# Performance work log

Hardware: AMD Instinct MI355X
Metric: run time of the kernel (lower is better)

## Reference

```python
import jax, jax.numpy as jnp
import numpy as np

WIN = 9  # window_size (isotropic, module default)
EPS = 1e-5


def _box_sum3d(x, win):
    """Sum over a win^3 box, same-size output ('same' padding). x: [B,1,D,H,W].
    The ones kernel is separable, so apply three 1D convolutions."""
    pad = win // 2
    for ax in range(3):  # spatial axes D,H,W
        kshape = [1, 1, 1, 1, 1]
        kshape[2 + ax] = win
        k = jnp.ones(kshape, x.dtype)
        padding = [(0, 0)] * 3
        padding[ax] = (pad, pad)
        x = jax.lax.conv_general_dilated(x, k, window_strides=(1, 1, 1), padding=padding)
    return x


def setup_inputs() -> dict:
    key = jax.random.key(0)
    k1, k2 = jax.random.split(key)
    shape = (2, 1, 160, 192, 160)
    y_pred = jax.random.normal(k1, shape, dtype=jnp.float32)
    y_true = jax.random.normal(k2, shape, dtype=jnp.float32)
    return {"y_pred": y_pred, "y_true": y_true}


def reference(y_pred, y_true):
    I, J = y_true, y_pred
    win_size = jnp.asarray(WIN ** 3, I.dtype)  # 729

    I_sum = _box_sum3d(I, WIN)
    J_sum = _box_sum3d(J, WIN)
    I2_sum = _box_sum3d(I * I, WIN)
    J2_sum = _box_sum3d(J * J, WIN)
    IJ_sum = _box_sum3d(I * J, WIN)

    I_mean = I_sum / win_size
    J_mean = J_sum / win_size

    cross = IJ_sum - J_mean * I_sum - I_mean * J_sum + I_mean * J_mean * win_size
    I_var = I2_sum - 2 * I_mean * I_sum + I_mean * I_mean * win_size
    J_var = J2_sum - 2 * J_mean * J_sum + J_mean * J_mean * win_size

    cc = cross * cross / (I_var * J_var + EPS)
    return -jnp.mean(cc)
```

## Files before the change

kernel.cpp:

```cpp
#include <hip/hip_runtime.h>


#define B_    2
#define D_    160
#define H_    192
#define W_    160
#define HW_   (H_*W_)
#define SSTR  28
#define SSLC  (24*SSTR)
#define OFF_J (2*SSLC)
#define WFS   484
#define OFF_WS 2688
#define HFS   324
#define OFF_HS (OFF_WS + 5*WFS)
#define OFF_RED (OFF_HS + 5*HFS)
#define SMEM_TOT (OFF_RED + 8)
#define DC    40
#define NMAC  24
#define W3I   (1.0f/729.0f)
#define NTOT  9830400.0f

#if __has_builtin(__builtin_amdgcn_rcpf)
#define RCP(x) __builtin_amdgcn_rcpf(x)
#else
#define RCP(x) (1.0f/(x))
#endif

#define LGKM0() asm volatile("s_waitcnt lgkmcnt(0)" ::: "memory")

#define SLIDEX(EXPR, F) { \
  float v_[12]; \
  _Pragma("unroll") for (int k_ = 0; k_ < 12; ++k_) { v_[k_] = (EXPR); } \
  float s_ = v_[0]+v_[1]+v_[2]+v_[3]+v_[4]+v_[5]+v_[6]+v_[7]+v_[8]; \
  float4 o_; o_.x = s_; s_ += v_[9]-v_[0]; o_.y = s_; \
  s_ += v_[10]-v_[1]; o_.z = s_; s_ += v_[11]-v_[2]; o_.w = s_; \
  *(float4*)&sm[wwr + (F)*WFS] = o_; }

__global__ __launch_bounds__(256, 4) void ncc_fused(const float* __restrict__ gI,
                                                    const float* __restrict__ gJ,
                                                    float* __restrict__ out)
{
  __shared__ __align__(16) float sm[SMEM_TOT];
  const int tid  = threadIdx.x;
  const int lane = tid & 63;
  const int Q    = tid >> 6;
  const int w0   = blockIdx.x * 16;
  const int h0   = blockIdx.y * 16;
  const int bz   = blockIdx.z;
  const int bb   = bz >> 2;
  const int d_lo = (bz & 3) * DC;

  for (int i = tid; i < OFF_WS; i += 256) sm[i] = 0.f;

  bool val0 = false, val1 = false;
  int  lds0 = 0, lds1 = 0, slc0 = 0, slc1 = 0;
  const float *pi0 = gI, *pj0 = gJ, *pi1 = gI, *pj1 = gJ;
  {
    const int tA = tid;
    const int tB = (tid >= 224) ? (tid + 32) : 512;
    auto prep = [&](int t, bool& val, int& lo, int& slc,
                    const float*& pi, const float*& pj) {
      if (t >= 288) { val = false; return; }
      slc = t / 144;
      const int u = t - slc*144;
      const int r = u / 6, c = u - r*6;
      const int gh = h0 - 4 + r;
      const int gw = w0 - 4 + 4*c;
      val = ((unsigned)gh < (unsigned)H_) && (gw >= 0) && (gw + 3 < W_);
      lo  = slc*SSLC + r*SSTR + 4*c;
      const long off = ((long)(bb*D_ + (d_lo - 4 + slc))*H_ + gh)*(long)W_ + gw;
      pi = gI + off; pj = gJ + off;
    };
    prep(tA, val0, lds0, slc0, pi0, pj0);
    prep(tB, val1, lds1, slc1, pi1, pj1);
  }

  const bool wact = (lane < 24);
  const int  wrd  = lane*SSTR + 4*Q;
  const int  wwr  = OFF_WS + lane*20 + 4*Q;

  const bool hact  = (lane < 40);
  const int  hwq   = lane & 3;
  const int  hf    = (lane >> 2) % 5;
  const int  hhalf = lane / 20;
  const int  hrd   = OFF_WS + hf*WFS + hhalf*160 + 4*Q + hwq;
  const int  hwr   = OFF_HS + hf*HFS + hhalf*160 + 4*Q + hwq;

  const int rh = lane >> 2, rwq = lane & 3;
  const int hb = OFF_HS + rh*20 + 4*Q + rwq;

  float ring[5][9], S[5];
  #pragma unroll
  for (int f = 0; f < 5; ++f) {
    S[f] = 0.f;
    #pragma unroll
    for (int k = 0; k < 9; ++k) ring[f][k] = 0.f;
  }
  float acc = 0.f;

  float4 f0i = {0,0,0,0}, f0j = {0,0,0,0}, f1i = {0,0,0,0}, f1j = {0,0,0,0};
  auto fetch = [&](int sbase) {
    if (val0 && (unsigned)(sbase + slc0) < (unsigned)D_) {
      f0i = *(const float4*)pi0; f0j = *(const float4*)pj0;
    } else { f0i = make_float4(0,0,0,0); f0j = make_float4(0,0,0,0); }
    pi0 += 2*HW_; pj0 += 2*HW_;
    if (val1 && (unsigned)(sbase + slc1) < (unsigned)D_) {
      f1i = *(const float4*)pi1; f1j = *(const float4*)pj1;
    } else { f1i = make_float4(0,0,0,0); f1j = make_float4(0,0,0,0); }
    pi1 += 2*HW_; pj1 += 2*HW_;
  };

  fetch(d_lo - 4);
  __syncthreads();
  if (val0) { *(float4*)&sm[lds0] = f0i; *(float4*)&sm[lds0 + OFF_J] = f0j; }
  if (val1) { *(float4*)&sm[lds1] = f1i; *(float4*)&sm[lds1 + OFF_J] = f1j; }
  __syncthreads();

  int sA = d_lo - 4;
  for (int m = 0; m < NMAC; ++m, sA += 2) {
    if (m + 1 < NMAC) fetch(sA + 2);

    #pragma unroll
    for (int slc = 0; slc < 2; ++slc) {
      if (wact) {
        const int rb = wrd + slc*SSLC;
        const float4 a0 = *(const float4*)&sm[rb];
        const float4 a1 = *(const float4*)&sm[rb + 4];
        const float4 a2 = *(const float4*)&sm[rb + 8];
        const float4 b0 = *(const float4*)&sm[rb + OFF_J];
        const float4 b1 = *(const float4*)&sm[rb + OFF_J + 4];
        const float4 b2 = *(const float4*)&sm[rb + OFF_J + 8];
        const float wi[12] = {a0.x,a0.y,a0.z,a0.w,a1.x,a1.y,a1.z,a1.w,a2.x,a2.y,a2.z,a2.w};
        const float wj[12] = {b0.x,b0.y,b0.z,b0.w,b1.x,b1.y,b1.z,b1.w,b2.x,b2.y,b2.z,b2.w};
        SLIDEX(wi[k_],        0)
        SLIDEX(wj[k_],        1)
        SLIDEX(wi[k_]*wi[k_], 2)
        SLIDEX(wj[k_]*wj[k_], 3)
        SLIDEX(wi[k_]*wj[k_], 4)
      }
      LGKM0();

      if (hact) {
        float v[16];
        #pragma unroll
        for (int k = 0; k < 16; ++k) v[k] = sm[hrd + k*20];
        float s = v[0]+v[1]+v[2]+v[3]+v[4]+v[5]+v[6]+v[7]+v[8];
        sm[hwr] = s;
        #pragma unroll
        for (int j = 1; j < 8; ++j) { s += v[j+8] - v[j-1]; sm[hwr + j*20] = s; }
      }
      LGKM0();

      {
        float nv[5];
        #pragma unroll
        for (int f = 0; f < 5; ++f) nv[f] = sm[hb + f*HFS];
        #pragma unroll
        for (int f = 0; f < 5; ++f) {
          S[f] += nv[f] - ring[f][8];
          #pragma unroll
          for (int k = 8; k > 0; --k) ring[f][k] = ring[f][k-1];
          ring[f][0] = nv[f];
        }
        if (m >= 4) {
          const float cr = S[4] - S[0]*S[1]*W3I;
          const float vi = S[2] - S[0]*S[0]*W3I;
          const float vj = S[3] - S[1]*S[1]*W3I;
          acc += cr*cr * RCP(vi*vj + 1e-5f);
        }
      }
      LGKM0();
    }

    __syncthreads();
    if (m + 1 < NMAC) {
      if (val0) { *(float4*)&sm[lds0] = f0i; *(float4*)&sm[lds0 + OFF_J] = f0j; }
      if (val1) { *(float4*)&sm[lds1] = f1i; *(float4*)&sm[lds1 + OFF_J] = f1j; }
    }
    __syncthreads();
  }

  float v = acc;
  #pragma unroll
  for (int off = 32; off > 0; off >>= 1)
    v += __shfl_down(v, off, 64);
  if (lane == 0) sm[OFF_RED + Q] = v;
  __syncthreads();
  if (tid == 0) {
    const float t = sm[OFF_RED] + sm[OFF_RED+1] + sm[OFF_RED+2] + sm[OFF_RED+3];
    atomicAdd(out, -t / NTOT);
  }
}

extern "C" void kernel_launch(void* const* d_in, const int* in_sizes, int n_in,
                              void* d_out, int out_size, void* d_ws, size_t ws_size,
                              hipStream_t stream) {
  const float* J = (const float*)d_in[0];
  const float* I = (const float*)d_in[1];
  float* outp = (float*)d_out;
  hipMemsetAsync(d_out, 0, sizeof(float), stream);
  dim3 grid(W_/16, H_/16, B_*4);
  ncc_fused<<<grid, dim3(256), 0, stream>>>(I, J, outp);
}
```

Before: 172.2 us.

## Process both staged slices together and defer depth-ring update one iteration

```diff
diff --git a/kernel.cpp b/kernel.cpp
--- a/kernel.cpp
+++ b/kernel.cpp
@@ -9,11 +9,13 @@
 #define SSTR  28
 #define SSLC  (24*SSTR)
 #define OFF_J (2*SSLC)
+#define OFF_WS 2688
 #define WFS   484
-#define OFF_WS 2688
+#define WSLC5 (5*WFS)
+#define OFF_HS (OFF_WS + 2*WSLC5)
 #define HFS   324
-#define OFF_HS (OFF_WS + 5*WFS)
-#define OFF_RED (OFF_HS + 5*HFS)
+#define HSLC5 (5*HFS)
+#define OFF_RED (OFF_HS + 2*HSLC5)
 #define SMEM_TOT (OFF_RED + 8)
 #define DC    40
 #define NMAC  24
@@ -36,7 +38,7 @@
   s_ += v_[10]-v_[1]; o_.z = s_; s_ += v_[11]-v_[2]; o_.w = s_; \
   *(float4*)&sm[wwr + (F)*WFS] = o_; }
 
-__global__ __launch_bounds__(256, 4) void ncc_fused(const float* __restrict__ gI,
+__global__ __launch_bounds__(256, 3) void ncc_fused(const float* __restrict__ gI,
                                                     const float* __restrict__ gJ,
                                                     float* __restrict__ out)
 {
@@ -75,19 +77,28 @@
     prep(tB, val1, lds1, slc1, pi1, pj1);
   }
 
-  const bool wact = (lane < 24);
-  const int  wrd  = lane*SSTR + 4*Q;
-  const int  wwr  = OFF_WS + lane*20 + 4*Q;
-
-  const bool hact  = (lane < 40);
-  const int  hwq   = lane & 3;
-  const int  hf    = (lane >> 2) % 5;
-  const int  hhalf = lane / 20;
-  const int  hrd   = OFF_WS + hf*WFS + hhalf*160 + 4*Q + hwq;
-  const int  hwr   = OFF_HS + hf*HFS + hhalf*160 + 4*Q + hwq;
+  const bool wact = (lane < 48);
+  const int  wslc = lane / 24;
+  const int  wrow = lane - wslc*24;
+  const int  wrd  = wslc*SSLC + wrow*SSTR + 4*Q;
+  const int  wwr  = OFF_WS + wslc*WSLC5 + wrow*20 + 4*Q;
+
+  auto prep_h = [&](int t, int& rd, int& wr) {
+    const int wq   = t & 3;
+    const int f    = (t >> 2) % 5;
+    const int half = (t / 20) & 1;
+    const int slc  = t / 40;
+    rd = OFF_WS + slc*WSLC5 + f*WFS + half*160 + 4*Q + wq;
+    wr = OFF_HS + slc*HSLC5 + f*HFS + half*160 + 4*Q + wq;
+  };
+  int h1rd, h1wr, h2rd = 0, h2wr = 0;
+  prep_h(lane, h1rd, h1wr);
+  const bool hact2 = (lane < 16);
+  if (hact2) prep_h(lane + 64, h2rd, h2wr);
 
   const int rh = lane >> 2, rwq = lane & 3;
-  const int hb = OFF_HS + rh*20 + 4*Q + rwq;
+  const int hbA = OFF_HS + rh*20 + 4*Q + rwq;
+  const int hbB = hbA + HSLC5;
 
   float ring[5][9], S[5];
   #pragma unroll
@@ -109,76 +120,89 @@
     } else { f1i = make_float4(0,0,0,0); f1j = make_float4(0,0,0,0); }
     pi1 += 2*HW_; pj1 += 2*HW_;
   };
+  auto stage_write = [&]() {
+    if (val0) { *(float4*)&sm[lds0] = f0i; *(float4*)&sm[lds0 + OFF_J] = f0j; }
+    if (val1) { *(float4*)&sm[lds1] = f1i; *(float4*)&sm[lds1 + OFF_J] = f1j; }
+  };
+
+  auto ring_cc = [&](int mu) {
+    float nA[5], nB[5];
+    #pragma unroll
+    for (int f = 0; f < 5; ++f) { nA[f] = sm[hbA + f*HFS]; nB[f] = sm[hbB + f*HFS]; }
+    float SA[5], SB[5];
+    #pragma unroll
+    for (int f = 0; f < 5; ++f) {
+      SA[f] = S[f]  + nA[f] - ring[f][8];
+      SB[f] = SA[f] + nB[f] - ring[f][7];
+      S[f]  = SB[f];
+      #pragma unroll
+      for (int k = 8; k >= 2; --k) ring[f][k] = ring[f][k-2];
+      ring[f][1] = nA[f]; ring[f][0] = nB[f];
+    }
+    if (mu >= 4) {
+      {
+        const float cr = SA[4] - SA[0]*SA[1]*W3I;
+        const float vi = SA[2] - SA[0]*SA[0]*W3I;
+        const float vj = SA[3] - SA[1]*SA[1]*W3I;
+        acc += cr*cr * RCP(vi*vj + 1e-5f);
+      }
+      {
+        const float cr = SB[4] - SB[0]*SB[1]*W3I;
+        const float vi = SB[2] - SB[0]*SB[0]*W3I;
+        const float vj = SB[3] - SB[1]*SB[1]*W3I;
+        acc += cr*cr * RCP(vi*vj + 1e-5f);
+      }
+    }
+  };
 
   fetch(d_lo - 4);
   __syncthreads();
-  if (val0) { *(float4*)&sm[lds0] = f0i; *(float4*)&sm[lds0 + OFF_J] = f0j; }
-  if (val1) { *(float4*)&sm[lds1] = f1i; *(float4*)&sm[lds1 + OFF_J] = f1j; }
+  stage_write();
   __syncthreads();
 
   int sA = d_lo - 4;
   for (int m = 0; m < NMAC; ++m, sA += 2) {
     if (m + 1 < NMAC) fetch(sA + 2);
 
-    #pragma unroll
-    for (int slc = 0; slc < 2; ++slc) {
-      if (wact) {
-        const int rb = wrd + slc*SSLC;
-        const float4 a0 = *(const float4*)&sm[rb];
-        const float4 a1 = *(const float4*)&sm[rb + 4];
-        const float4 a2 = *(const float4*)&sm[rb + 8];
-        const float4 b0 = *(const float4*)&sm[rb + OFF_J];
-        const float4 b1 = *(const float4*)&sm[rb + OFF_J + 4];
-        const float4 b2 = *(const float4*)&sm[rb + OFF_J + 8];
-        const float wi[12] = {a0.x,a0.y,a0.z,a0.w,a1.x,a1.y,a1.z,a1.w,a2.x,a2.y,a2.z,a2.w};
-        const float wj[12] = {b0.x,b0.y,b0.z,b0.w,b1.x,b1.y,b1.z,b1.w,b2.x,b2.y,b2.z,b2.w};
-        SLIDEX(wi[k_],        0)
-        SLIDEX(wj[k_],        1)
-        SLIDEX(wi[k_]*wi[k_], 2)
-        SLIDEX(wj[k_]*wj[k_], 3)
-        SLIDEX(wi[k_]*wj[k_], 4)
-      }
-      LGKM0();
-
-      if (hact) {
+    if (m > 0) ring_cc(m - 1);
+
+    if (wact) {
+      const float4 a0 = *(const float4*)&sm[wrd];
+      const float4 a1 = *(const float4*)&sm[wrd + 4];
+      const float4 a2 = *(const float4*)&sm[wrd + 8];
+      const float4 b0 = *(const float4*)&sm[wrd + OFF_J];
+      const float4 b1 = *(const float4*)&sm[wrd + OFF_J + 4];
+      const float4 b2 = *(const float4*)&sm[wrd + OFF_J + 8];
+      const float wi[12] = {a0.x,a0.y,a0.z,a0.w,a1.x,a1.y,a1.z,a1.w,a2.x,a2.y,a2.z,a2.w};
+      const float wj[12] = {b0.x,b0.y,b0.z,b0.w,b1.x,b1.y,b1.z,b1.w,b2.x,b2.y,b2.z,b2.w};
+      SLIDEX(wi[k_],        0)
+      SLIDEX(wj[k_],        1)
+      SLIDEX(wi[k_]*wi[k_], 2)
+      SLIDEX(wj[k_]*wj[k_], 3)
+      SLIDEX(wi[k_]*wj[k_], 4)
+    }
+    LGKM0();
+
+    {
+      auto hrun = [&](int rd, int wr) {
         float v[16];
         #pragma unroll
-        for (int k = 0; k < 16; ++k) v[k] = sm[hrd + k*20];
+        for (int k = 0; k < 16; ++k) v[k] = sm[rd + k*20];
         float s = v[0]+v[1]+v[2]+v[3]+v[4]+v[5]+v[6]+v[7]+v[8];
-        sm[hwr] = s;
+        sm[wr] = s;
         #pragma unroll
-        for (int j = 1; j < 8; ++j) { s += v[j+8] - v[j-1]; sm[hwr + j*20] = s; }
-      }
-      LGKM0();
-
-      {
-        float nv[5];
-        #pragma unroll
-        for (int f = 0; f < 5; ++f) nv[f] = sm[hb + f*HFS];
-        #pragma unroll
-        for (int f = 0; f < 5; ++f) {
-          S[f] += nv[f] - ring[f][8];
-          #pragma unroll
-          for (int k = 8; k > 0; --k) ring[f][k] = ring[f][k-1];
-          ring[f][0] = nv[f];
-        }
-        if (m >= 4) {
-          const float cr = S[4] - S[0]*S[1]*W3I;
-          const float vi = S[2] - S[0]*S[0]*W3I;
-          const float vj = S[3] - S[1]*S[1]*W3I;
-          acc += cr*cr * RCP(vi*vj + 1e-5f);
-        }
-      }
-      LGKM0();
+        for (int j = 1; j < 8; ++j) { s += v[j+8] - v[j-1]; sm[wr + j*20] = s; }
+      };
+      hrun(h1rd, h1wr);
+      if (hact2) hrun(h2rd, h2wr);
     }
 
     __syncthreads();
-    if (m + 1 < NMAC) {
-      if (val0) { *(float4*)&sm[lds0] = f0i; *(float4*)&sm[lds0 + OFF_J] = f0j; }
-      if (val1) { *(float4*)&sm[lds1] = f1i; *(float4*)&sm[lds1 + OFF_J] = f1j; }
-    }
+    if (m + 1 < NMAC) stage_write();
     __syncthreads();
   }
+
+  ring_cc(NMAC - 1);
 
   float v = acc;
   #pragma unroll
```

After: 174.6 us. Within noise of the previous version (+1.4%).
